# Performance work log

Hardware: AMD Instinct MI355X
Metric: run time of the kernel (lower is better)

Reference implementation:

```python
import jax, jax.numpy as jnp
import numpy as np

L_TOK = 16384   # token sequence length
L_CHK = 8192    # number of chunks (True entries in boundary_mask)
HIDDEN = 4096


def setup_inputs() -> dict:
    key = jax.random.key(0)
    k1, k2 = jax.random.split(key)
    concept = jax.random.normal(k1, (1, L_CHK, HIDDEN), dtype=jnp.float32)
    # keep probs strictly inside (0,1) like real router probs
    selected_probs = jax.random.uniform(k2, (1, L_TOK, 1), dtype=jnp.float32,
                                        minval=0.05, maxval=0.95)
    # every 2nd token is a chunk boundary; first token must be a boundary
    boundary_mask = (jnp.arange(L_TOK) % 2 == 0)[None, :]  # [1, L_TOK], L_CHK True
    return {"concept": concept, "selected_probs": selected_probs,
            "boundary_mask": boundary_mask}


def reference(concept, selected_probs, boundary_mask):
    # concept: [1, Lc, H]; selected_probs: [1, L, 1]; boundary_mask: [1, L] bool
    Lc = concept.shape[1]
    idx = jnp.nonzero(boundary_mask[0], size=Lc)[0]        # [Lc] boundary token ids
    p = selected_probs[0, idx, 0]                          # [Lc]

    # EMA recurrence: y_0 = concept_0; y_i = y_{i-1}*(1-p_i) + concept_i*p_i
    a = (1.0 - p)[:, None]                                 # [Lc, 1]
    a = a.at[0].set(0.0)
    b = concept[0] * p[:, None]                            # [Lc, H]
    b = b.at[0].set(concept[0, 0])

    def combine(e1, e2):
        a1, b1 = e1
        a2, b2 = e2
        return (a1 * a2, b1 * a2 + b2)

    _, merge = jax.lax.associative_scan(combine, (a, b))   # [Lc, H]

    # plug merged chunk states back to every token of its chunk
    plug_back_idx = jnp.cumsum(boundary_mask[0].astype(jnp.int32)) - 1  # [L]
    return merge[plug_back_idx][None]                      # [1, L, H]
```

## Files before the change

### kernel.cpp

```cpp
#include <hip/hip_runtime.h>

typedef float f32x4 __attribute__((ext_vector_type(4)));


#define SEG 16
#define TPB 256
#define SETUP_T 1024

__global__ void __launch_bounds__(SETUP_T)
setup_kernel(const unsigned char* __restrict__ mask,
             const float* __restrict__ probs,
             float* __restrict__ A, float* __restrict__ Pc,
             int* __restrict__ start, int L, int Lc) {
    __shared__ int flag;
    __shared__ int wsum[SETUP_T / 64];
    const int t = threadIdx.x;
    const int lane = t & 63, wv = t >> 6;
    if (t == 0) flag = 0;
    __syncthreads();

    int4 v8 = ((const int4*)mask)[t];
    int f = (v8.x & (int)0xFFFFFF00) | (v8.y & (int)0xFFFFFF00) |
            (v8.z & (int)0xFFFFFF00) | (v8.w & (int)0xFFFFFF00);
    if (f) atomicOr(&flag, 1);
    __syncthreads();
    const bool isU8 = (flag != 0);

    unsigned mbits = 0;
    if (isU8) {
        unsigned dw[4] = {(unsigned)v8.x, (unsigned)v8.y, (unsigned)v8.z, (unsigned)v8.w};
#pragma unroll
        for (int q = 0; q < 4; ++q)
#pragma unroll
            for (int b = 0; b < 4; ++b)
                if ((dw[q] >> (8 * b)) & 0xFFu) mbits |= 1u << (q * 4 + b);
    } else {
        const int4* m4 = (const int4*)mask;
#pragma unroll
        for (int q = 0; q < 4; ++q) {
            int4 w = m4[t * 4 + q];
            if (w.x) mbits |= 1u << (q * 4 + 0);
            if (w.y) mbits |= 1u << (q * 4 + 1);
            if (w.z) mbits |= 1u << (q * 4 + 2);
            if (w.w) mbits |= 1u << (q * 4 + 3);
        }
    }
    int c = __popc(mbits);

    int s = c;
#pragma unroll
    for (int off = 1; off < 64; off <<= 1) {
        int v = __shfl_up(s, off, 64);
        if (lane >= off) s += v;
    }
    if (lane == 63) wsum[wv] = s;
    __syncthreads();
    if (t == 0) {
        int acc = 0;
        for (int w = 0; w < SETUP_T / 64; ++w) { int x = wsum[w]; wsum[w] = acc; acc += x; }
    }
    __syncthreads();

    int rank = wsum[wv] + (s - c);
    const int t0 = t * 16;
#pragma unroll
    for (int k = 0; k < 16; ++k) {
        if ((mbits >> k) & 1u) {
            if (rank < Lc) {
                int tok = t0 + k;
                start[rank] = tok;
                float p = probs[tok];
                A[rank]  = (rank == 0) ? 0.0f : (1.0f - p);
                Pc[rank] = (rank == 0) ? 1.0f : p;
            }
            rank++;
        }
    }
    if (t == 0) start[Lc] = L;
}

__global__ void __launch_bounds__(TPB)
segsum_kernel(const float* __restrict__ cpt,
              const float* __restrict__ A, const float* __restrict__ Pc,
              float* __restrict__ Bend, float* __restrict__ Aseg,
              int H, int CG) {
    const int g  = blockIdx.x / CG;
    const int cg = blockIdx.x % CG;
    const int ch = cg * (TPB * 4) + threadIdx.x * 4;
    const int i0 = g * SEG;

    __shared__ float sA[SEG], sP[SEG];
    if (threadIdx.x < SEG) { sA[threadIdx.x] = A[i0 + threadIdx.x]; sP[threadIdx.x] = Pc[i0 + threadIdx.x]; }
    __syncthreads();

    const int strideF4 = H / 4;
    const f32x4* cp = (const f32x4*)(cpt + (size_t)i0 * H + ch);
    f32x4 y = {0.f, 0.f, 0.f, 0.f};
    float pa = 1.0f;
#pragma unroll 8
    for (int k = 0; k < SEG; ++k) {
        const float a = sA[k], p = sP[k];
        f32x4 c = cp[(size_t)k * strideF4];
        y = a * y + p * c;
        pa *= a;
    }
    *(f32x4*)(Bend + (size_t)g * H + ch) = y;
    if (threadIdx.x == 0 && cg == 0) Aseg[g] = pa;
}

__global__ void __launch_bounds__(TPB)
scan_write_kernel(const float* __restrict__ cpt,
                  const float* __restrict__ A, const float* __restrict__ Pc,
                  const int* __restrict__ start,
                  const float* __restrict__ Bend, const float* __restrict__ Aseg,
                  float* __restrict__ out, int H, int CG) {
    const int g  = blockIdx.x / CG;
    const int cg = blockIdx.x % CG;
    const int ch = cg * (TPB * 4) + threadIdx.x * 4;
    const int i0 = g * SEG;

    __shared__ float sA[SEG], sP[SEG];
    __shared__ int   sS[SEG + 1];
    if (threadIdx.x < SEG)     { sA[threadIdx.x] = A[i0 + threadIdx.x]; sP[threadIdx.x] = Pc[i0 + threadIdx.x]; }
    if (threadIdx.x < SEG + 1) { sS[threadIdx.x] = start[i0 + threadIdx.x]; }
    __syncthreads();

    const int strideF4 = H / 4;
    const f32x4* cp = (const f32x4*)(cpt + (size_t)i0 * H + ch);
    f32x4 c[SEG];
#pragma unroll
    for (int k = 0; k < SEG; ++k) c[k] = cp[(size_t)k * strideF4];

    f32x4 y = {0.f, 0.f, 0.f, 0.f};
    {
        float w = 1.0f;
        for (int j = g - 1; j >= 0; --j) {
            f32x4 b = *(const f32x4*)(Bend + (size_t)j * H + ch);
            y += w * b;
            w *= Aseg[j];
            if (w < 1e-10f) break;
        }
    }

#pragma unroll
    for (int k = 0; k < SEG; ++k) {
        y = sA[k] * y + sP[k] * c[k];
        const int ts = sS[k], te = sS[k + 1];
        for (int t = ts; t < te; ++t) {
            __builtin_nontemporal_store(y, (f32x4*)(out + (size_t)t * H + ch));
        }
    }
}

extern "C" void kernel_launch(void* const* d_in, const int* in_sizes, int n_in,
                              void* d_out, int out_size, void* d_ws, size_t ws_size,
                              hipStream_t stream) {
    const float* cpt   = (const float*)d_in[0];
    const float* probs = (const float*)d_in[1];
    const unsigned char* mask = (const unsigned char*)d_in[2];

    const int L  = in_sizes[1];
    const int H  = out_size / L;
    const int Lc = in_sizes[0] / H;
    const int G  = Lc / SEG;
    const int CG = H / (TPB * 4);

    char* ws = (char*)d_ws;
    size_t off = 0;
    auto alloc = [&](size_t bytes) {
        size_t o = off;
        off += (bytes + 255) & ~(size_t)255;
        return (void*)(ws + o);
    };
    float* A     = (float*)alloc((size_t)Lc * 4);
    float* Pc    = (float*)alloc((size_t)Lc * 4);
    int*   start = (int*)  alloc((size_t)(Lc + 1) * 4);
    float* Aseg  = (float*)alloc((size_t)G * 4);
    float* Bend  = (float*)alloc((size_t)G * H * 4);
    (void)ws_size;

    hipLaunchKernelGGL(setup_kernel, dim3(1), dim3(SETUP_T), 0, stream,
                       mask, probs, A, Pc, start, L, Lc);
    hipLaunchKernelGGL(segsum_kernel, dim3(G * CG), dim3(TPB), 0, stream,
                       cpt, A, Pc, Bend, Aseg, H, CG);
    hipLaunchKernelGGL(scan_write_kernel, dim3(G * CG), dim3(TPB), 0, stream,
                       cpt, A, Pc, start, Bend, Aseg, (float*)d_out, H, CG);
}
```

Before: 105.2 us.

## Fuse segment-sum pass into scan by recomputing carry-in from decayed prior concepts

Removes the segsum kernel and its Bend/Aseg buffers. Each block now rebuilds its carry-in state directly from preceding concept rows, weighting each row by a cumulative decay product that one wavefront computes 64 rows at a time with a shuffle-based product scan. It stops once the weight falls below a tolerance. This saves a kernel launch and the intermediate write and read, at the cost of extra concept reads per block, which can be several rows deep for probabilities near 0.05.

```diff
diff --git a/kernel.cpp b/kernel.cpp
--- a/kernel.cpp
+++ b/kernel.cpp
@@ -6,6 +6,7 @@
 #define SEG 16
 #define TPB 256
 #define SETUP_T 1024
+#define TOL 1e-12f
 
 __global__ void __launch_bounds__(SETUP_T)
 setup_kernel(const unsigned char* __restrict__ mask,
@@ -80,39 +81,9 @@
 }
 
 __global__ void __launch_bounds__(TPB)
-segsum_kernel(const float* __restrict__ cpt,
-              const float* __restrict__ A, const float* __restrict__ Pc,
-              float* __restrict__ Bend, float* __restrict__ Aseg,
-              int H, int CG) {
-    const int g  = blockIdx.x / CG;
-    const int cg = blockIdx.x % CG;
-    const int ch = cg * (TPB * 4) + threadIdx.x * 4;
-    const int i0 = g * SEG;
-
-    __shared__ float sA[SEG], sP[SEG];
-    if (threadIdx.x < SEG) { sA[threadIdx.x] = A[i0 + threadIdx.x]; sP[threadIdx.x] = Pc[i0 + threadIdx.x]; }
-    __syncthreads();
-
-    const int strideF4 = H / 4;
-    const f32x4* cp = (const f32x4*)(cpt + (size_t)i0 * H + ch);
-    f32x4 y = {0.f, 0.f, 0.f, 0.f};
-    float pa = 1.0f;
-#pragma unroll 8
-    for (int k = 0; k < SEG; ++k) {
-        const float a = sA[k], p = sP[k];
-        f32x4 c = cp[(size_t)k * strideF4];
-        y = a * y + p * c;
-        pa *= a;
-    }
-    *(f32x4*)(Bend + (size_t)g * H + ch) = y;
-    if (threadIdx.x == 0 && cg == 0) Aseg[g] = pa;
-}
-
-__global__ void __launch_bounds__(TPB)
-scan_write_kernel(const float* __restrict__ cpt,
+scan_fused_kernel(const float* __restrict__ cpt,
                   const float* __restrict__ A, const float* __restrict__ Pc,
                   const int* __restrict__ start,
-                  const float* __restrict__ Bend, const float* __restrict__ Aseg,
                   float* __restrict__ out, int H, int CG) {
     const int g  = blockIdx.x / CG;
     const int cg = blockIdx.x % CG;
@@ -121,9 +92,11 @@
 
     __shared__ float sA[SEG], sP[SEG];
     __shared__ int   sS[SEG + 1];
+    __shared__ float tcoef[64];
+    __shared__ float sh_wnext;
+    __shared__ int   sh_nt;
     if (threadIdx.x < SEG)     { sA[threadIdx.x] = A[i0 + threadIdx.x]; sP[threadIdx.x] = Pc[i0 + threadIdx.x]; }
     if (threadIdx.x < SEG + 1) { sS[threadIdx.x] = start[i0 + threadIdx.x]; }
-    __syncthreads();
 
     const int strideF4 = H / 4;
     const f32x4* cp = (const f32x4*)(cpt + (size_t)i0 * H + ch);
@@ -132,15 +105,40 @@
     for (int k = 0; k < SEG; ++k) c[k] = cp[(size_t)k * strideF4];
 
     f32x4 y = {0.f, 0.f, 0.f, 0.f};
-    {
-        float w = 1.0f;
-        for (int j = g - 1; j >= 0; --j) {
-            f32x4 b = *(const f32x4*)(Bend + (size_t)j * H + ch);
-            y += w * b;
-            w *= Aseg[j];
-            if (w < 1e-10f) break;
+    int jw = i0 - 1;
+    float wbase = 1.0f;
+    while (jw >= 0) {
+        if (threadIdx.x < 64) {
+            const int lane = threadIdx.x;
+            const int j = jw - lane;
+            const float a = (j >= 0) ? A[j]  : 0.0f;
+            const float p = (j >= 0) ? Pc[j] : 0.0f;
+            float s = a;
+#pragma unroll
+            for (int off = 1; off < 64; off <<= 1) {
+                float v = __shfl_up(s, off, 64);
+                if (lane >= off) s *= v;
+            }
+            float E = __shfl_up(s, 1, 64);
+            if (lane == 0) E = 1.0f;
+            E *= wbase;
+            tcoef[lane] = E * p;
+            if (lane == 63) sh_wnext = E * a;
+            unsigned long long bal = __ballot(E < TOL);
+            if (lane == 0) sh_nt = bal ? (__ffsll((long long)bal) - 1) : 64;
         }
+        __syncthreads();
+        const int nt = min(min(64, jw + 1), sh_nt);
+        const f32x4* bp = (const f32x4*)(cpt + (size_t)jw * H + ch);
+        for (int t = 0; t < nt; ++t) {
+            y += tcoef[t] * bp[-(size_t)t * strideF4];
+        }
+        if (sh_nt < 64 || jw < 64) break;
+        wbase = sh_wnext;
+        jw -= 64;
+        __syncthreads();
     }
+    __syncthreads();
 
 #pragma unroll
     for (int k = 0; k < SEG; ++k) {
@@ -175,14 +173,10 @@
     float* A     = (float*)alloc((size_t)Lc * 4);
     float* Pc    = (float*)alloc((size_t)Lc * 4);
     int*   start = (int*)  alloc((size_t)(Lc + 1) * 4);
-    float* Aseg  = (float*)alloc((size_t)G * 4);
-    float* Bend  = (float*)alloc((size_t)G * H * 4);
     (void)ws_size;
 
     hipLaunchKernelGGL(setup_kernel, dim3(1), dim3(SETUP_T), 0, stream,
                        mask, probs, A, Pc, start, L, Lc);
-    hipLaunchKernelGGL(segsum_kernel, dim3(G * CG), dim3(TPB), 0, stream,
-                       cpt, A, Pc, Bend, Aseg, H, CG);
-    hipLaunchKernelGGL(scan_write_kernel, dim3(G * CG), dim3(TPB), 0, stream,
-                       cpt, A, Pc, start, Bend, Aseg, (float*)d_out, H, CG);
+    hipLaunchKernelGGL(scan_fused_kernel, dim3(G * CG), dim3(TPB), 0, stream,
+                       cpt, A, Pc, start, (float*)d_out, H, CG);
 }
```

Result: slower. 121.3 us (+15.4%).

## Fuse segment-sum and scan-write into single-pass decoupled lookback kernel

Applied to the files above, without the earlier changes.

Merges the two scan kernels into one kernel that computes each segment's local aggregate, publishes it with a release flag, then looks back over earlier segments using acquire spin-waits before writing output. Blocks take a dynamic ticket so predecessors are scheduled first, and setup now zeroes the flags and ticket. This avoids reading the concept tensor twice and drops one launch, at the cost of inter-block synchronisation and spin latency.

```diff
diff --git a/kernel.cpp b/kernel.cpp
--- a/kernel.cpp
+++ b/kernel.cpp
@@ -6,16 +6,22 @@
 #define SEG 16
 #define TPB 256
 #define SETUP_T 1024
+#define TOL 1e-10f
 
 __global__ void __launch_bounds__(SETUP_T)
 setup_kernel(const unsigned char* __restrict__ mask,
              const float* __restrict__ probs,
              float* __restrict__ A, float* __restrict__ Pc,
-             int* __restrict__ start, int L, int Lc) {
+             int* __restrict__ start,
+             int* __restrict__ flags, int nzero,
+             int L, int Lc) {
     __shared__ int flag;
     __shared__ int wsum[SETUP_T / 64];
     const int t = threadIdx.x;
     const int lane = t & 63, wv = t >> 6;
+
+    for (int i = t; i < nzero; i += SETUP_T) flags[i] = 0;
+
     if (t == 0) flag = 0;
     __syncthreads();
 
@@ -80,66 +86,63 @@
 }
 
 __global__ void __launch_bounds__(TPB)
-segsum_kernel(const float* __restrict__ cpt,
-              const float* __restrict__ A, const float* __restrict__ Pc,
-              float* __restrict__ Bend, float* __restrict__ Aseg,
-              int H, int CG) {
-    const int g  = blockIdx.x / CG;
-    const int cg = blockIdx.x % CG;
+scan_fused_kernel(const float* __restrict__ cpt,
+                  const float* __restrict__ A, const float* __restrict__ Pc,
+                  const int* __restrict__ start,
+                  float* __restrict__ Bend, float* __restrict__ Aseg,
+                  int* __restrict__ flags, int* __restrict__ ticket,
+                  float* __restrict__ out, int H, int CG) {
+    __shared__ int sh_blk;
+    __shared__ float sA[SEG], sP[SEG];
+    __shared__ int   sS[SEG + 1];
+
+    if (threadIdx.x == 0) sh_blk = atomicAdd(ticket, 1);
+    __syncthreads();
+    const int blk = sh_blk;
+    const int g  = blk / CG;
+    const int cg = blk % CG;
     const int ch = cg * (TPB * 4) + threadIdx.x * 4;
     const int i0 = g * SEG;
 
-    __shared__ float sA[SEG], sP[SEG];
-    if (threadIdx.x < SEG) { sA[threadIdx.x] = A[i0 + threadIdx.x]; sP[threadIdx.x] = Pc[i0 + threadIdx.x]; }
-    __syncthreads();
-
-    const int strideF4 = H / 4;
-    const f32x4* cp = (const f32x4*)(cpt + (size_t)i0 * H + ch);
-    f32x4 y = {0.f, 0.f, 0.f, 0.f};
-    float pa = 1.0f;
-#pragma unroll 8
-    for (int k = 0; k < SEG; ++k) {
-        const float a = sA[k], p = sP[k];
-        f32x4 c = cp[(size_t)k * strideF4];
-        y = a * y + p * c;
-        pa *= a;
-    }
-    *(f32x4*)(Bend + (size_t)g * H + ch) = y;
-    if (threadIdx.x == 0 && cg == 0) Aseg[g] = pa;
-}
-
-__global__ void __launch_bounds__(TPB)
-scan_write_kernel(const float* __restrict__ cpt,
-                  const float* __restrict__ A, const float* __restrict__ Pc,
-                  const int* __restrict__ start,
-                  const float* __restrict__ Bend, const float* __restrict__ Aseg,
-                  float* __restrict__ out, int H, int CG) {
-    const int g  = blockIdx.x / CG;
-    const int cg = blockIdx.x % CG;
-    const int ch = cg * (TPB * 4) + threadIdx.x * 4;
-    const int i0 = g * SEG;
-
-    __shared__ float sA[SEG], sP[SEG];
-    __shared__ int   sS[SEG + 1];
     if (threadIdx.x < SEG)     { sA[threadIdx.x] = A[i0 + threadIdx.x]; sP[threadIdx.x] = Pc[i0 + threadIdx.x]; }
     if (threadIdx.x < SEG + 1) { sS[threadIdx.x] = start[i0 + threadIdx.x]; }
-    __syncthreads();
 
     const int strideF4 = H / 4;
     const f32x4* cp = (const f32x4*)(cpt + (size_t)i0 * H + ch);
     f32x4 c[SEG];
 #pragma unroll
     for (int k = 0; k < SEG; ++k) c[k] = cp[(size_t)k * strideF4];
+    __syncthreads();
+
+    f32x4 B = {0.f, 0.f, 0.f, 0.f};
+    float pa = 1.0f;
+#pragma unroll
+    for (int k = 0; k < SEG; ++k) {
+        B = sA[k] * B + sP[k] * c[k];
+        pa *= sA[k];
+    }
+    *(f32x4*)(Bend + (size_t)blk * (TPB * 4) + threadIdx.x * 4) = B;
+    if (threadIdx.x == 0) Aseg[blk] = pa;
+    __threadfence();
+    __syncthreads();
+    if (threadIdx.x == 0)
+        __hip_atomic_store(flags + blk, 1, __ATOMIC_RELEASE, __HIP_MEMORY_SCOPE_AGENT);
 
     f32x4 y = {0.f, 0.f, 0.f, 0.f};
-    {
-        float w = 1.0f;
-        for (int j = g - 1; j >= 0; --j) {
-            f32x4 b = *(const f32x4*)(Bend + (size_t)j * H + ch);
-            y += w * b;
-            w *= Aseg[j];
-            if (w < 1e-10f) break;
+    float w = 1.0f;
+    for (int j = g - 1; j >= 0; --j) {
+        const int cell = j * CG + cg;
+        if (threadIdx.x == 0) {
+            while (__hip_atomic_load(flags + cell, __ATOMIC_ACQUIRE,
+                                     __HIP_MEMORY_SCOPE_AGENT) == 0) {
+                __builtin_amdgcn_s_sleep(1);
+            }
         }
+        __syncthreads();
+        f32x4 b = *(const f32x4*)(Bend + (size_t)cell * (TPB * 4) + threadIdx.x * 4);
+        y += w * b;
+        w *= Aseg[cell];
+        if (w < TOL) break;
     }
 
 #pragma unroll
@@ -164,6 +167,7 @@
     const int Lc = in_sizes[0] / H;
     const int G  = Lc / SEG;
     const int CG = H / (TPB * 4);
+    const int NC = G * CG;
 
     char* ws = (char*)d_ws;
     size_t off = 0;
@@ -175,14 +179,15 @@
     float* A     = (float*)alloc((size_t)Lc * 4);
     float* Pc    = (float*)alloc((size_t)Lc * 4);
     int*   start = (int*)  alloc((size_t)(Lc + 1) * 4);
-    float* Aseg  = (float*)alloc((size_t)G * 4);
-    float* Bend  = (float*)alloc((size_t)G * H * 4);
+    float* Aseg  = (float*)alloc((size_t)NC * 4);
+    int*   flags = (int*)  alloc((size_t)NC * 4);
+    int*   tkt   = (int*)  alloc(256);
+    float* Bend  = (float*)alloc((size_t)NC * TPB * 4 * 4);
     (void)ws_size;
 
     hipLaunchKernelGGL(setup_kernel, dim3(1), dim3(SETUP_T), 0, stream,
-                       mask, probs, A, Pc, start, L, Lc);
-    hipLaunchKernelGGL(segsum_kernel, dim3(G * CG), dim3(TPB), 0, stream,
-                       cpt, A, Pc, Bend, Aseg, H, CG);
-    hipLaunchKernelGGL(scan_write_kernel, dim3(G * CG), dim3(TPB), 0, stream,
-                       cpt, A, Pc, start, Bend, Aseg, (float*)d_out, H, CG);
+                       mask, probs, A, Pc, start, flags, NC + 64, L, Lc);
+    hipLaunchKernelGGL(scan_fused_kernel, dim3(NC), dim3(TPB), 0, stream,
+                       cpt, A, Pc, start, Bend, Aseg, flags, tkt,
+                       (float*)d_out, H, CG);
 }
```

New measurement: 403.2 us. +283.4%, slower.

## Fuse mask decoding into segment kernels and drop the single-block setup kernel

Applied to the files above, without the earlier changes.

Removes the single-block setup kernel that built the start, A and Pc arrays. Instead, every block of the segsum and scan_write kernels re-decodes the full boundary mask with 256 threads covering 64 tokens each, computes prefix ranks, and keeps only the 16 chunks of its own segment in shared memory. Concept loads are issued before the decode so their latency can overlap it. This saves one launch and the serial setup step, but every block now redundantly reads the whole mask and executes extra syncs and scalar work.

```diff
diff --git a/kernel.cpp b/kernel.cpp
--- a/kernel.cpp
+++ b/kernel.cpp
@@ -5,115 +5,135 @@
 
 #define SEG 16
 #define TPB 256
-#define SETUP_T 1024
-
-__global__ void __launch_bounds__(SETUP_T)
-setup_kernel(const unsigned char* __restrict__ mask,
-             const float* __restrict__ probs,
-             float* __restrict__ A, float* __restrict__ Pc,
-             int* __restrict__ start, int L, int Lc) {
-    __shared__ int flag;
-    __shared__ int wsum[SETUP_T / 64];
+#define TOL 1e-10f
+
+__device__ __forceinline__ void decode_segment(
+    const unsigned char* __restrict__ mask,
+    const float* __restrict__ probs,
+    int L, int Lc, int i0,
+    float* sA, float* sP, int* sS, int* sScr )
+{
     const int t = threadIdx.x;
     const int lane = t & 63, wv = t >> 6;
-    if (t == 0) flag = 0;
-    __syncthreads();
-
-    int4 v8 = ((const int4*)mask)[t];
-    int f = (v8.x & (int)0xFFFFFF00) | (v8.y & (int)0xFFFFFF00) |
-            (v8.z & (int)0xFFFFFF00) | (v8.w & (int)0xFFFFFF00);
-    if (f) atomicOr(&flag, 1);
-    __syncthreads();
-    const bool isU8 = (flag != 0);
-
-    unsigned mbits = 0;
+    if (t == 0) sScr[4] = 0;
+    __syncthreads();
+
+    int4 v[4];
+    const int4* m16 = (const int4*)mask;
+#pragma unroll
+    for (int q = 0; q < 4; ++q) v[q] = m16[t * 4 + q];
+    int f = 0;
+#pragma unroll
+    for (int q = 0; q < 4; ++q)
+        f |= (v[q].x & (int)0xFFFFFF00) | (v[q].y & (int)0xFFFFFF00) |
+             (v[q].z & (int)0xFFFFFF00) | (v[q].w & (int)0xFFFFFF00);
+    if (f) atomicOr(&sScr[4], 1);
+    __syncthreads();
+    const bool isU8 = (sScr[4] != 0);
+
+    unsigned long long mb = 0ULL;
     if (isU8) {
-        unsigned dw[4] = {(unsigned)v8.x, (unsigned)v8.y, (unsigned)v8.z, (unsigned)v8.w};
-#pragma unroll
-        for (int q = 0; q < 4; ++q)
-#pragma unroll
-            for (int b = 0; b < 4; ++b)
-                if ((dw[q] >> (8 * b)) & 0xFFu) mbits |= 1u << (q * 4 + b);
+#pragma unroll
+        for (int q = 0; q < 4; ++q) {
+            const unsigned dw[4] = {(unsigned)v[q].x, (unsigned)v[q].y,
+                                    (unsigned)v[q].z, (unsigned)v[q].w};
+#pragma unroll
+            for (int d = 0; d < 4; ++d)
+#pragma unroll
+                for (int b = 0; b < 4; ++b)
+                    if ((dw[d] >> (8 * b)) & 0xFFu)
+                        mb |= 1ULL << (q * 16 + d * 4 + b);
+        }
     } else {
         const int4* m4 = (const int4*)mask;
 #pragma unroll
-        for (int q = 0; q < 4; ++q) {
-            int4 w = m4[t * 4 + q];
-            if (w.x) mbits |= 1u << (q * 4 + 0);
-            if (w.y) mbits |= 1u << (q * 4 + 1);
-            if (w.z) mbits |= 1u << (q * 4 + 2);
-            if (w.w) mbits |= 1u << (q * 4 + 3);
-        }
-    }
-    int c = __popc(mbits);
-
+        for (int q = 0; q < 16; ++q) {
+            int4 w = m4[t * 16 + q];
+            if (w.x) mb |= 1ULL << (q * 4 + 0);
+            if (w.y) mb |= 1ULL << (q * 4 + 1);
+            if (w.z) mb |= 1ULL << (q * 4 + 2);
+            if (w.w) mb |= 1ULL << (q * 4 + 3);
+        }
+    }
+
+    const int c = __popcll(mb);
     int s = c;
 #pragma unroll
     for (int off = 1; off < 64; off <<= 1) {
-        int v = __shfl_up(s, off, 64);
-        if (lane >= off) s += v;
-    }
-    if (lane == 63) wsum[wv] = s;
-    __syncthreads();
-    if (t == 0) {
-        int acc = 0;
-        for (int w = 0; w < SETUP_T / 64; ++w) { int x = wsum[w]; wsum[w] = acc; acc += x; }
-    }
-    __syncthreads();
-
-    int rank = wsum[wv] + (s - c);
-    const int t0 = t * 16;
-#pragma unroll
-    for (int k = 0; k < 16; ++k) {
-        if ((mbits >> k) & 1u) {
-            if (rank < Lc) {
-                int tok = t0 + k;
-                start[rank] = tok;
-                float p = probs[tok];
-                A[rank]  = (rank == 0) ? 0.0f : (1.0f - p);
-                Pc[rank] = (rank == 0) ? 1.0f : p;
+        int vv = __shfl_up(s, off, 64);
+        if (lane >= off) s += vv;
+    }
+    if (lane == 63) sScr[wv] = s;
+    __syncthreads();
+    const int w0 = sScr[0], w1 = sScr[1], w2 = sScr[2];
+    const int rank0 = ((wv > 0) ? w0 : 0) + ((wv > 1) ? w1 : 0) +
+                      ((wv > 2) ? w2 : 0) + (s - c);
+    __syncthreads();
+
+    if (t == 0 && i0 + SEG >= Lc) sS[SEG] = L;
+
+    const int lo = i0, hi = i0 + SEG;
+    if (rank0 <= hi && rank0 + c > lo) {
+        unsigned long long m = mb;
+        int r = rank0;
+        while (m && r <= hi) {
+            const int b = __ffsll((unsigned long long)m) - 1;
+            m &= m - 1;
+            if (r >= lo) {
+                const int token = t * 64 + b;
+                sS[r - lo] = token;
+                if (r < hi) {
+                    const float p = probs[token];
+                    sA[r - lo] = (r == 0) ? 0.0f : 1.0f - p;
+                    sP[r - lo] = (r == 0) ? 1.0f : p;
+                }
             }
-            rank++;
-        }
-    }
-    if (t == 0) start[Lc] = L;
+            ++r;
+        }
+    }
+    __syncthreads();
 }
 
 __global__ void __launch_bounds__(TPB)
 segsum_kernel(const float* __restrict__ cpt,
-              const float* __restrict__ A, const float* __restrict__ Pc,
+              const unsigned char* __restrict__ mask,
+              const float* __restrict__ probs,
               float* __restrict__ Bend, float* __restrict__ Aseg,
-              int H, int CG) {
+              int H, int CG, int L, int Lc) {
     const int g  = blockIdx.x / CG;
     const int cg = blockIdx.x % CG;
     const int ch = cg * (TPB * 4) + threadIdx.x * 4;
     const int i0 = g * SEG;
 
     __shared__ float sA[SEG], sP[SEG];
-    if (threadIdx.x < SEG) { sA[threadIdx.x] = A[i0 + threadIdx.x]; sP[threadIdx.x] = Pc[i0 + threadIdx.x]; }
-    __syncthreads();
+    __shared__ int   sS[SEG + 1];
+    __shared__ int   sScr[8];
 
     const int strideF4 = H / 4;
     const f32x4* cp = (const f32x4*)(cpt + (size_t)i0 * H + ch);
-    f32x4 y = {0.f, 0.f, 0.f, 0.f};
+    f32x4 c[SEG];
+#pragma unroll
+    for (int k = 0; k < SEG; ++k) c[k] = cp[(size_t)k * strideF4];
+
+    decode_segment(mask, probs, L, Lc, i0, sA, sP, sS, sScr);
+
+    f32x4 B = {0.f, 0.f, 0.f, 0.f};
     float pa = 1.0f;
-#pragma unroll 8
+#pragma unroll
     for (int k = 0; k < SEG; ++k) {
-        const float a = sA[k], p = sP[k];
-        f32x4 c = cp[(size_t)k * strideF4];
-        y = a * y + p * c;
-        pa *= a;
-    }
-    *(f32x4*)(Bend + (size_t)g * H + ch) = y;
+        B = sA[k] * B + sP[k] * c[k];
+        pa *= sA[k];
+    }
+    *(f32x4*)(Bend + (size_t)g * H + ch) = B;
     if (threadIdx.x == 0 && cg == 0) Aseg[g] = pa;
 }
 
 __global__ void __launch_bounds__(TPB)
 scan_write_kernel(const float* __restrict__ cpt,
-                  const float* __restrict__ A, const float* __restrict__ Pc,
-                  const int* __restrict__ start,
+                  const unsigned char* __restrict__ mask,
+                  const float* __restrict__ probs,
                   const float* __restrict__ Bend, const float* __restrict__ Aseg,
-                  float* __restrict__ out, int H, int CG) {
+                  float* __restrict__ out, int H, int CG, int L, int Lc) {
     const int g  = blockIdx.x / CG;
     const int cg = blockIdx.x % CG;
     const int ch = cg * (TPB * 4) + threadIdx.x * 4;
@@ -121,15 +141,15 @@
 
     __shared__ float sA[SEG], sP[SEG];
     __shared__ int   sS[SEG + 1];
-    if (threadIdx.x < SEG)     { sA[threadIdx.x] = A[i0 + threadIdx.x]; sP[threadIdx.x] = Pc[i0 + threadIdx.x]; }
-    if (threadIdx.x < SEG + 1) { sS[threadIdx.x] = start[i0 + threadIdx.x]; }
-    __syncthreads();
+    __shared__ int   sScr[8];
 
     const int strideF4 = H / 4;
     const f32x4* cp = (const f32x4*)(cpt + (size_t)i0 * H + ch);
     f32x4 c[SEG];
 #pragma unroll
     for (int k = 0; k < SEG; ++k) c[k] = cp[(size_t)k * strideF4];
+
+    decode_segment(mask, probs, L, Lc, i0, sA, sP, sS, sScr);
 
     f32x4 y = {0.f, 0.f, 0.f, 0.f};
     {
@@ -138,7 +158,7 @@
             f32x4 b = *(const f32x4*)(Bend + (size_t)j * H + ch);
             y += w * b;
             w *= Aseg[j];
-            if (w < 1e-10f) break;
+            if (w < TOL) break;
         }
     }
 
@@ -172,17 +192,12 @@
         off += (bytes + 255) & ~(size_t)255;
         return (void*)(ws + o);
     };
-    float* A     = (float*)alloc((size_t)Lc * 4);
-    float* Pc    = (float*)alloc((size_t)Lc * 4);
-    int*   start = (int*)  alloc((size_t)(Lc + 1) * 4);
-    float* Aseg  = (float*)alloc((size_t)G * 4);
-    float* Bend  = (float*)alloc((size_t)G * H * 4);
+    float* Aseg = (float*)alloc((size_t)G * 4);
+    float* Bend = (float*)alloc((size_t)G * H * 4);
     (void)ws_size;
 
-    hipLaunchKernelGGL(setup_kernel, dim3(1), dim3(SETUP_T), 0, stream,
-                       mask, probs, A, Pc, start, L, Lc);
     hipLaunchKernelGGL(segsum_kernel, dim3(G * CG), dim3(TPB), 0, stream,
-                       cpt, A, Pc, Bend, Aseg, H, CG);
+                       cpt, mask, probs, Bend, Aseg, H, CG, L, Lc);
     hipLaunchKernelGGL(scan_write_kernel, dim3(G * CG), dim3(TPB), 0, stream,
-                       cpt, A, Pc, start, Bend, Aseg, (float*)d_out, H, CG);
-}
+                       cpt, mask, probs, Bend, Aseg, (float*)d_out, H, CG, L, Lc);
+}
```

After: 116.3 us. 1.11x slower.
